# Optimization experiments

Hardware: AMD Instinct MI355X
Metric: run time of the kernel (lower is better)

The kernel has to match this reference:

```python
import jax, jax.numpy as jnp
import numpy as np
import math

B, H, L, D = 2, 16, 2048, 128

def setup_inputs() -> dict:
    key = jax.random.key(0)
    kq, kk, kv, km = jax.random.split(key, 4)
    q = jax.random.normal(kq, (B, H, L, D), dtype=jnp.float32)
    k = jax.random.normal(kk, (B, H, L, D), dtype=jnp.float32)
    v = jax.random.normal(kv, (B, H, L, D), dtype=jnp.float32)
    mask = jax.random.randint(km, (B, 1, L, L), 0, 2, dtype=jnp.int32)
    return {"q": q, "k": k, "v": v, "mask": mask}

def reference(q, k, v, mask):
    d_tensor = q.shape[-1]
    # ReLU applied to V before attention (the custom twist)
    v = jax.nn.relu(v)
    # score = q @ k^T / sqrt(d)  -> [B,H,L,L]
    score = jnp.einsum('bhqd,bhkd->bhqk', q, k) / math.sqrt(d_tensor)
    score = jnp.where(mask == 0, jnp.float32(-10000.0), score)
    attn = jax.nn.softmax(score, axis=-1)
    # result = attn @ relu(v) -> [B,H,L,D]
    return jnp.einsum('bhqk,bhkd->bhqd', attn, v)
```

## Files before the change

### kernel.cpp

```cpp
#include <hip/hip_runtime.h>
#include <hip/hip_bf16.h>
#include <math.h>

typedef __attribute__((ext_vector_type(8)))  short short8;
typedef __attribute__((ext_vector_type(16))) float f32x16;

#define Bc    2
#define Hc    16
#define Lc    2048
#define Dc    128
#define QBLK  128
#define KBLK  64
#define LOG2E 1.4426950408889634f
#define SCALE 0.08838834764831845f
#define SCL2  (SCALE * LOG2E)

#define KB_OFF   0u
#define KB_BYTES (32u * 2048u * 128u * 2u)
#define VT_OFF   (KB_OFF + KB_BYTES)
#define VT_BYTES (32u * 2048u * 128u * 2u)
#define MB_OFF   (VT_OFF + VT_BYTES)

__device__ __forceinline__ unsigned pk2(float a, float b) {
    unsigned short ua = __builtin_bit_cast(unsigned short, __float2bfloat16(a));
    unsigned short ub = __builtin_bit_cast(unsigned short, __float2bfloat16(b));
    return (unsigned)ua | ((unsigned)ub << 16);
}
__device__ __forceinline__ unsigned short bf16b(float a) {
    return __builtin_bit_cast(unsigned short, __float2bfloat16(a));
}
__device__ __forceinline__ void gload_lds16(const void* g, void* l) {
    __builtin_amdgcn_global_load_lds(
        (const __attribute__((address_space(1))) unsigned int*)g,
        (__attribute__((address_space(3))) unsigned int*)l, 16, 0, 0);
}
__device__ __forceinline__ unsigned cvtpk(float lo, float hi) {
    unsigned r;
    asm("v_cvt_pk_bf16_f32 %0, %1, %2" : "=v"(r) : "v"(lo), "v"(hi));
    return r;
}

__global__ void conv_k_kernel(const float* __restrict__ k, unsigned short* __restrict__ kb) {
    int idx8 = blockIdx.x * 256 + threadIdx.x;
    size_t base = (size_t)idx8 * 8;
    float4 f0 = *(const float4*)(k + base);
    float4 f1 = *(const float4*)(k + base + 4);
    uint4 w;
    w.x = pk2(f0.x, f0.y); w.y = pk2(f0.z, f0.w);
    w.z = pk2(f1.x, f1.y); w.w = pk2(f1.z, f1.w);
    *(uint4*)(kb + base) = w;
}

__global__ void transp_v_kernel(const float* __restrict__ v, unsigned short* __restrict__ vt) {
    __shared__ float t[32][33];
    int d0 = blockIdx.x * 32;
    int l0 = blockIdx.y * 32;
    int bh = blockIdx.z;
    int tx = threadIdx.x, ty = threadIdx.y;
    const float* src = v + (size_t)bh * Lc * Dc;
    unsigned short* dst = vt + (size_t)bh * Dc * Lc;
    #pragma unroll
    for (int i = 0; i < 4; ++i) {
        int row = ty * 4 + i;
        t[row][tx] = fmaxf(src[(size_t)(l0 + row) * Dc + d0 + tx], 0.f);
    }
    __syncthreads();
    #pragma unroll
    for (int i = 0; i < 4; ++i) {
        int drow = ty * 4 + i;
        dst[(size_t)(d0 + drow) * Lc + l0 + tx] = bf16b(t[tx][drow]);
    }
}

__global__ void mask_pack_kernel(const int* __restrict__ mask, unsigned long long* __restrict__ mb) {
    int tid  = threadIdx.x;
    int wv   = blockIdx.x * 4 + (tid >> 6);
    int lane = tid & 63;
    int b    = wv >> 16;
    int l    = (wv >> 5) & 2047;
    int ktw  = wv & 31;
    int m = mask[(((size_t)(b * 2048 + l)) << 11) + ktw * 64 + lane];
    unsigned long long bal = __ballot(m != 0);
    if (lane == 0) mb[(((size_t)(b * 32 + ktw)) << 11) + l] = bal;
}

__global__ __launch_bounds__(256, 2) void rev_attn_kernel(
    const float* __restrict__ q,
    const unsigned short* __restrict__ kb,
    const unsigned short* __restrict__ vt,
    const unsigned long long* __restrict__ mb,
    float* __restrict__ out)
{
    __shared__ __align__(16) char smem[65536];

    const int tid  = threadIdx.x;
    const int w    = tid >> 6;
    const int lane = tid & 63;
    const int l31  = lane & 31;
    const int hi   = lane >> 5;
    const int bh   = blockIdx.y;
    const int b    = bh >> 4;
    const int qb   = blockIdx.x * QBLK + w * 32;
    const int qrow = qb + l31;

    const float*              qp = q  + (size_t)bh * Lc * Dc;
    const unsigned short*     kp = kb + (size_t)bh * Lc * Dc;
    const unsigned short*     vp = vt + (size_t)bh * Dc * Lc;
    const unsigned long long* mp = mb + ((size_t)b << 16);
    float*                    op = out + (size_t)bh * Lc * Dc;

    short8 qf[8];
    {
        const float* qr0 = qp + (size_t)qrow * Dc + hi * 8;
        #pragma unroll
        for (int c = 0; c < 8; ++c) {
            const float* src = qr0 + c * 16;
            #pragma unroll
            for (int j = 0; j < 8; ++j)
                qf[c][j] = (short)bf16b(src[j] * SCL2);
        }
    }

    f32x16 o0 = (f32x16)0.f, o1 = (f32x16)0.f, o2 = (f32x16)0.f, o3 = (f32x16)0.f;
    f32x16 lacc = (f32x16)0.f;
    short8 ones;
    #pragma unroll
    for (int j = 0; j < 8; ++j) ones[j] = (short)0x3F80;

    #define STAGE(buf, kt_) do {                                                   \
        char* Kdst = smem + (buf) * 16384;                                         \
        char* Vdst = smem + 32768 + (buf) * 16384;                                 \
        _Pragma("unroll")                                                          \
        for (int p = 0; p < 4; ++p) {                                              \
            int l   = p * 256 + tid;                                               \
            int row = l >> 4, cl = l & 15;                                         \
            int s_  = cl ^ (row & 15);                                             \
            gload_lds16(kp + (size_t)((kt_) + row) * Dc + s_ * 8, Kdst + l * 16);  \
            int ds_ = row + ((s_ >> 3) << 6);                                      \
            int ko_ = (s_ & 7) * 8;                                                \
            gload_lds16(vp + (size_t)ds_ * Lc + (kt_) + ko_, Vdst + l * 16);       \
        }                                                                          \
    } while (0)

    int cur = 0;
    STAGE(0, 0);
    __syncthreads();

    for (int kt = 0; kt < Lc; kt += KBLK) {
        if (kt + KBLK < Lc) STAGE(cur ^ 1, kt + KBLK);
        unsigned long long mw = mp[((size_t)(kt >> 6) << 11) + qrow];
        const char* Kb = smem + cur * 16384;
        const char* Vb = smem + 32768 + cur * 16384;

        f32x16 s0 = (f32x16)0.f, s1 = (f32x16)0.f;
        __builtin_amdgcn_s_setprio(1);
        #pragma unroll
        for (int c = 0; c < 8; ++c) {
            int r0 = l31;
            short8 kf0 = *(const short8*)(Kb + r0 * 256 + ((((c << 1) | hi)) ^ (r0 & 15)) * 16);
            s0 = __builtin_amdgcn_mfma_f32_32x32x16_bf16(kf0, qf[c], s0, 0, 0, 0);
            int r1 = 32 + l31;
            short8 kf1 = *(const short8*)(Kb + r1 * 256 + ((((c << 1) | hi)) ^ (r1 & 15)) * 16);
            s1 = __builtin_amdgcn_mfma_f32_32x32x16_bf16(kf1, qf[c], s1, 0, 0, 0);
        }
        __builtin_amdgcn_s_setprio(0);

        unsigned m0 = ((unsigned)(mw & 0xffffffffull)) >> (4 * hi);
        unsigned m1 = ((unsigned)(mw >> 32)) >> (4 * hi);
        #pragma unroll
        for (int r = 0; r < 16; ++r) {
            const int cs = (r & 3) + 8 * (r >> 2);
            float e0 = exp2f(s0[r]);
            float e1 = exp2f(s1[r]);
            s0[r] = ((m0 >> cs) & 1u) ? e0 : 0.f;
            s1[r] = ((m1 >> cs) & 1u) ? e1 : 0.f;
        }

        short8 pa[4];
        {
            union { unsigned u[4]; short8 v; } t0, t1, t2, t3;
            unsigned a, a2, bb, b2;
            a  = cvtpk(s0[0], s0[1]);  a2 = cvtpk(s0[2], s0[3]);
            bb = cvtpk(s0[4], s0[5]);  b2 = cvtpk(s0[6], s0[7]);
            asm volatile("v_permlane32_swap_b32 %0, %1" : "+v"(a),  "+v"(bb));
            asm volatile("v_permlane32_swap_b32 %0, %1" : "+v"(a2), "+v"(b2));
            t0.u[0] = a; t0.u[1] = a2; t0.u[2] = bb; t0.u[3] = b2;
            a  = cvtpk(s0[8],  s0[9]);  a2 = cvtpk(s0[10], s0[11]);
            bb = cvtpk(s0[12], s0[13]); b2 = cvtpk(s0[14], s0[15]);
            asm volatile("v_permlane32_swap_b32 %0, %1" : "+v"(a),  "+v"(bb));
            asm volatile("v_permlane32_swap_b32 %0, %1" : "+v"(a2), "+v"(b2));
            t1.u[0] = a; t1.u[1] = a2; t1.u[2] = bb; t1.u[3] = b2;
            a  = cvtpk(s1[0], s1[1]);  a2 = cvtpk(s1[2], s1[3]);
            bb = cvtpk(s1[4], s1[5]);  b2 = cvtpk(s1[6], s1[7]);
            asm volatile("v_permlane32_swap_b32 %0, %1" : "+v"(a),  "+v"(bb));
            asm volatile("v_permlane32_swap_b32 %0, %1" : "+v"(a2), "+v"(b2));
            t2.u[0] = a; t2.u[1] = a2; t2.u[2] = bb; t2.u[3] = b2;
            a  = cvtpk(s1[8],  s1[9]);  a2 = cvtpk(s1[10], s1[11]);
            bb = cvtpk(s1[12], s1[13]); b2 = cvtpk(s1[14], s1[15]);
            asm volatile("v_permlane32_swap_b32 %0, %1" : "+v"(a),  "+v"(bb));
            asm volatile("v_permlane32_swap_b32 %0, %1" : "+v"(a2), "+v"(b2));
            t3.u[0] = a; t3.u[1] = a2; t3.u[2] = bb; t3.u[3] = b2;
            pa[0] = t0.v; pa[1] = t1.v; pa[2] = t2.v; pa[3] = t3.v;
        }

        __builtin_amdgcn_s_setprio(1);
        #pragma unroll
        for (int ks = 0; ks < 4; ++ks)
            lacc = __builtin_amdgcn_mfma_f32_32x32x16_bf16(ones, pa[ks], lacc, 0, 0, 0);
        #pragma unroll
        for (int dt = 0; dt < 4; ++dt) {
            int vrow = (dt & 1) * 32 + l31;
            int hs   = dt >> 1;
            int vswz = vrow & 15;
            f32x16 acc = (dt == 0) ? o0 : (dt == 1) ? o1 : (dt == 2) ? o2 : o3;
            #pragma unroll
            for (int ks = 0; ks < 4; ++ks) {
                int off = vrow * 256 + (((hs << 3) | (ks << 1) | hi) ^ vswz) * 16;
                short8 vf = *(const short8*)(Vb + off);
                acc = __builtin_amdgcn_mfma_f32_32x32x16_bf16(vf, pa[ks], acc, 0, 0, 0);
            }
            if (dt == 0) o0 = acc; else if (dt == 1) o1 = acc; else if (dt == 2) o2 = acc; else o3 = acc;
        }
        __builtin_amdgcn_s_setprio(0);

        __syncthreads();
        cur ^= 1;
    }

    __syncthreads();
    float inv = 1.0f / lacc[0];
    float* scr = (float*)(smem + w * 4608);
    const int qq = lane >> 1;
    const int dh = (lane & 1) * 16;
    #pragma unroll
    for (int dt = 0; dt < 4; ++dt) {
        const f32x16& oo = (dt == 0) ? o0 : (dt == 1) ? o1 : (dt == 2) ? o2 : o3;
        #pragma unroll
        for (int r = 0; r < 16; ++r) {
            int drow = (r & 3) + 8 * (r >> 2) + 4 * hi;
            scr[drow * 36 + l31] = oo[r] * inv;
        }
        asm volatile("s_waitcnt lgkmcnt(0)" ::: "memory");
        __builtin_amdgcn_sched_barrier(0);
        float t[16];
        #pragma unroll
        for (int c2 = 0; c2 < 16; ++c2)
            t[c2] = scr[(dh + c2) * 36 + qq];
        asm volatile("s_waitcnt lgkmcnt(0)" ::: "memory");
        __builtin_amdgcn_sched_barrier(0);
        float* od = op + (size_t)(qb + qq) * Dc + dt * 32 + dh;
        #pragma unroll
        for (int c2 = 0; c2 < 4; ++c2) {
            float4 f4; f4.x = t[c2*4]; f4.y = t[c2*4+1]; f4.z = t[c2*4+2]; f4.w = t[c2*4+3];
            *(float4*)(od + c2 * 4) = f4;
        }
    }
}

extern "C" void kernel_launch(void* const* d_in, const int* in_sizes, int n_in,
                              void* d_out, int out_size, void* d_ws, size_t ws_size,
                              hipStream_t stream) {
    const float* q    = (const float*)d_in[0];
    const float* k    = (const float*)d_in[1];
    const float* v    = (const float*)d_in[2];
    const int*   mask = (const int*)d_in[3];
    float*       out  = (float*)d_out;

    char* ws = (char*)d_ws;
    unsigned short*     kb  = (unsigned short*)(ws + KB_OFF);
    unsigned short*     vt  = (unsigned short*)(ws + VT_OFF);
    unsigned long long* mbp = (unsigned long long*)(ws + MB_OFF);

    hipLaunchKernelGGL(conv_k_kernel, dim3(4096), dim3(256), 0, stream, k, kb);
    hipLaunchKernelGGL(transp_v_kernel, dim3(4, 64, 32), dim3(32, 8), 0, stream, v, vt);
    hipLaunchKernelGGL(mask_pack_kernel, dim3(32768), dim3(256), 0, stream, mask, mbp);

    hipLaunchKernelGGL(rev_attn_kernel, dim3(Lc / QBLK, Bc * Hc), dim3(256), 0, stream,
                       q, kb, vt, mbp, out);
}
```

Baseline: 130.9 us.

## Split each key tile across wave pairs and compute row sums with VALU

Each block now runs 512 threads (8 waves). Pairs of waves share the same 32 query rows, and each wave handles one 32-key half of every 64-key tile, for both QK^T and PV. The row-sum MFMA against a ones vector is replaced by VALU adds plus a cross-half shuffle. At the end, partial O and l are combined through LDS before normalisation and the store. The aim is more waves in flight for latency hiding and shorter per-wave dependency chains. The cost is an extra LDS reduction with several block barriers, and register pressure from the tighter launch bounds.

New measurement: 244.0 us. 1.86x slower.

```diff
diff --git a/kernel.cpp b/kernel.cpp
--- a/kernel.cpp
+++ b/kernel.cpp
@@ -84,7 +84,7 @@
     if (lane == 0) mb[(((size_t)(b * 32 + ktw)) << 11) + l] = bal;
 }
 
-__global__ __launch_bounds__(256, 2) void rev_attn_kernel(
+__global__ __launch_bounds__(512, 4) void rev_attn_kernel(
     const float* __restrict__ q,
     const unsigned short* __restrict__ kb,
     const unsigned short* __restrict__ vt,
@@ -98,10 +98,12 @@
     const int lane = tid & 63;
     const int l31  = lane & 31;
     const int hi   = lane >> 5;
+    const int qg   = w >> 1;
+    const int kh   = w & 1;
     const int bh   = blockIdx.y;
     const int b    = bh >> 4;
-    const int qb   = blockIdx.x * QBLK + w * 32;
-    const int qrow = qb + l31;
+    const int qb   = blockIdx.x * QBLK;
+    const int qrow = qb + qg * 32 + l31;
 
     const float*              qp = q  + (size_t)bh * Lc * Dc;
     const unsigned short*     kp = kb + (size_t)bh * Lc * Dc;
@@ -122,17 +124,14 @@
     }
 
     f32x16 o0 = (f32x16)0.f, o1 = (f32x16)0.f, o2 = (f32x16)0.f, o3 = (f32x16)0.f;
-    f32x16 lacc = (f32x16)0.f;
-    short8 ones;
-    #pragma unroll
-    for (int j = 0; j < 8; ++j) ones[j] = (short)0x3F80;
+    float lrun = 0.f;
 
     #define STAGE(buf, kt_) do {                                                   \
         char* Kdst = smem + (buf) * 16384;                                         \
         char* Vdst = smem + 32768 + (buf) * 16384;                                 \
         _Pragma("unroll")                                                          \
-        for (int p = 0; p < 4; ++p) {                                              \
-            int l   = p * 256 + tid;                                               \
+        for (int p = 0; p < 2; ++p) {                                              \
+            int l   = p * 512 + tid;                                               \
             int row = l >> 4, cl = l & 15;                                         \
             int s_  = cl ^ (row & 15);                                             \
             gload_lds16(kp + (size_t)((kt_) + row) * Dc + s_ * 8, Kdst + l * 16);  \
@@ -146,67 +145,59 @@
     STAGE(0, 0);
     __syncthreads();
 
+    const int r0 = kh * 32 + l31;
     for (int kt = 0; kt < Lc; kt += KBLK) {
         if (kt + KBLK < Lc) STAGE(cur ^ 1, kt + KBLK);
         unsigned long long mw = mp[((size_t)(kt >> 6) << 11) + qrow];
         const char* Kb = smem + cur * 16384;
         const char* Vb = smem + 32768 + cur * 16384;
 
-        f32x16 s0 = (f32x16)0.f, s1 = (f32x16)0.f;
+        f32x16 s = (f32x16)0.f;
         __builtin_amdgcn_s_setprio(1);
         #pragma unroll
         for (int c = 0; c < 8; ++c) {
-            int r0 = l31;
-            short8 kf0 = *(const short8*)(Kb + r0 * 256 + ((((c << 1) | hi)) ^ (r0 & 15)) * 16);
-            s0 = __builtin_amdgcn_mfma_f32_32x32x16_bf16(kf0, qf[c], s0, 0, 0, 0);
-            int r1 = 32 + l31;
-            short8 kf1 = *(const short8*)(Kb + r1 * 256 + ((((c << 1) | hi)) ^ (r1 & 15)) * 16);
-            s1 = __builtin_amdgcn_mfma_f32_32x32x16_bf16(kf1, qf[c], s1, 0, 0, 0);
+            short8 kf = *(const short8*)(Kb + r0 * 256 + ((((c << 1) | hi)) ^ (r0 & 15)) * 16);
+            s = __builtin_amdgcn_mfma_f32_32x32x16_bf16(kf, qf[c], s, 0, 0, 0);
         }
         __builtin_amdgcn_s_setprio(0);
 
-        unsigned m0 = ((unsigned)(mw & 0xffffffffull)) >> (4 * hi);
-        unsigned m1 = ((unsigned)(mw >> 32)) >> (4 * hi);
+        unsigned mh = (unsigned)(mw >> (kh * 32));
+        unsigned m0 = mh >> (4 * hi);
         #pragma unroll
         for (int r = 0; r < 16; ++r) {
             const int cs = (r & 3) + 8 * (r >> 2);
-            float e0 = exp2f(s0[r]);
-            float e1 = exp2f(s1[r]);
-            s0[r] = ((m0 >> cs) & 1u) ? e0 : 0.f;
-            s1[r] = ((m1 >> cs) & 1u) ? e1 : 0.f;
-        }
-
-        short8 pa[4];
+            float e = exp2f(s[r]);
+            s[r] = ((m0 >> cs) & 1u) ? e : 0.f;
+        }
+
         {
-            union { unsigned u[4]; short8 v; } t0, t1, t2, t3;
+            float a0 = (s[0] + s[1]) + (s[2] + s[3]);
+            float a1 = (s[4] + s[5]) + (s[6] + s[7]);
+            float a2 = (s[8] + s[9]) + (s[10] + s[11]);
+            float a3 = (s[12] + s[13]) + (s[14] + s[15]);
+            float rs = (a0 + a1) + (a2 + a3);
+            rs += __shfl_xor(rs, 32);
+            lrun += rs;
+        }
+
+        short8 pa[2];
+        {
+            union { unsigned u[4]; short8 v; } t0, t1;
             unsigned a, a2, bb, b2;
-            a  = cvtpk(s0[0], s0[1]);  a2 = cvtpk(s0[2], s0[3]);
-            bb = cvtpk(s0[4], s0[5]);  b2 = cvtpk(s0[6], s0[7]);
+            a  = cvtpk(s[0], s[1]);  a2 = cvtpk(s[2], s[3]);
+            bb = cvtpk(s[4], s[5]);  b2 = cvtpk(s[6], s[7]);
             asm volatile("v_permlane32_swap_b32 %0, %1" : "+v"(a),  "+v"(bb));
             asm volatile("v_permlane32_swap_b32 %0, %1" : "+v"(a2), "+v"(b2));
             t0.u[0] = a; t0.u[1] = a2; t0.u[2] = bb; t0.u[3] = b2;
-            a  = cvtpk(s0[8],  s0[9]);  a2 = cvtpk(s0[10], s0[11]);
-            bb = cvtpk(s0[12], s0[13]); b2 = cvtpk(s0[14], s0[15]);
+            a  = cvtpk(s[8],  s[9]);  a2 = cvtpk(s[10], s[11]);
+            bb = cvtpk(s[12], s[13]); b2 = cvtpk(s[14], s[15]);
             asm volatile("v_permlane32_swap_b32 %0, %1" : "+v"(a),  "+v"(bb));
             asm volatile("v_permlane32_swap_b32 %0, %1" : "+v"(a2), "+v"(b2));
             t1.u[0] = a; t1.u[1] = a2; t1.u[2] = bb; t1.u[3] = b2;
-            a  = cvtpk(s1[0], s1[1]);  a2 = cvtpk(s1[2], s1[3]);
-            bb = cvtpk(s1[4], s1[5]);  b2 = cvtpk(s1[6], s1[7]);
-            asm volatile("v_permlane32_swap_b32 %0, %1" : "+v"(a),  "+v"(bb));
-            asm volatile("v_permlane32_swap_b32 %0, %1" : "+v"(a2), "+v"(b2));
-            t2.u[0] = a; t2.u[1] = a2; t2.u[2] = bb; t2.u[3] = b2;
-            a  = cvtpk(s1[8],  s1[9]);  a2 = cvtpk(s1[10], s1[11]);
-            bb = cvtpk(s1[12], s1[13]); b2 = cvtpk(s1[14], s1[15]);
-            asm volatile("v_permlane32_swap_b32 %0, %1" : "+v"(a),  "+v"(bb));
-            asm volatile("v_permlane32_swap_b32 %0, %1" : "+v"(a2), "+v"(b2));
-            t3.u[0] = a; t3.u[1] = a2; t3.u[2] = bb; t3.u[3] = b2;
-            pa[0] = t0.v; pa[1] = t1.v; pa[2] = t2.v; pa[3] = t3.v;
+            pa[0] = t0.v; pa[1] = t1.v;
         }
 
         __builtin_amdgcn_s_setprio(1);
-        #pragma unroll
-        for (int ks = 0; ks < 4; ++ks)
-            lacc = __builtin_amdgcn_mfma_f32_32x32x16_bf16(ones, pa[ks], lacc, 0, 0, 0);
         #pragma unroll
         for (int dt = 0; dt < 4; ++dt) {
             int vrow = (dt & 1) * 32 + l31;
@@ -214,9 +205,9 @@
             int vswz = vrow & 15;
             f32x16 acc = (dt == 0) ? o0 : (dt == 1) ? o1 : (dt == 2) ? o2 : o3;
             #pragma unroll
-            for (int ks = 0; ks < 4; ++ks) {
-                int off = vrow * 256 + (((hs << 3) | (ks << 1) | hi) ^ vswz) * 16;
-                short8 vf = *(const short8*)(Vb + off);
+            for (int ks = 0; ks < 2; ++ks) {
+                int colsel = (hs << 3) | (kh << 2) | (ks << 1) | hi;
+                short8 vf = *(const short8*)(Vb + vrow * 256 + ((colsel ^ vswz) * 16));
                 acc = __builtin_amdgcn_mfma_f32_32x32x16_bf16(vf, pa[ks], acc, 0, 0, 0);
             }
             if (dt == 0) o0 = acc; else if (dt == 1) o1 = acc; else if (dt == 2) o2 = acc; else o3 = acc;
@@ -227,33 +218,41 @@
         cur ^= 1;
     }
 
-    __syncthreads();
-    float inv = 1.0f / lacc[0];
-    float* scr = (float*)(smem + w * 4608);
-    const int qq = lane >> 1;
-    const int dh = (lane & 1) * 16;
+    float* scr = (float*)(smem + qg * 4096);
+    float* lsp = (float*)(smem + 16384 + qg * 128);
+    if (kh == 1 && hi == 0) lsp[l31] = lrun;
+    float inv = 0.f;
+    const int qq2 = kh * 16 + (lane >> 2);
+    const int dh2 = (lane & 3) * 8;
     #pragma unroll
     for (int dt = 0; dt < 4; ++dt) {
         const f32x16& oo = (dt == 0) ? o0 : (dt == 1) ? o1 : (dt == 2) ? o2 : o3;
-        #pragma unroll
-        for (int r = 0; r < 16; ++r) {
-            int drow = (r & 3) + 8 * (r >> 2) + 4 * hi;
-            scr[drow * 36 + l31] = oo[r] * inv;
-        }
-        asm volatile("s_waitcnt lgkmcnt(0)" ::: "memory");
-        __builtin_amdgcn_sched_barrier(0);
-        float t[16];
-        #pragma unroll
-        for (int c2 = 0; c2 < 16; ++c2)
-            t[c2] = scr[(dh + c2) * 36 + qq];
-        asm volatile("s_waitcnt lgkmcnt(0)" ::: "memory");
-        __builtin_amdgcn_sched_barrier(0);
-        float* od = op + (size_t)(qb + qq) * Dc + dt * 32 + dh;
-        #pragma unroll
-        for (int c2 = 0; c2 < 4; ++c2) {
-            float4 f4; f4.x = t[c2*4]; f4.y = t[c2*4+1]; f4.z = t[c2*4+2]; f4.w = t[c2*4+3];
-            *(float4*)(od + c2 * 4) = f4;
-        }
+        if (kh == 1) {
+            #pragma unroll
+            for (int r = 0; r < 16; ++r)
+                scr[((r & 3) + 8 * (r >> 2) + 4 * hi) * 32 + l31] = oo[r];
+        }
+        __syncthreads();
+        if (kh == 0) {
+            if (dt == 0) inv = 1.0f / (lrun + lsp[l31]);
+            #pragma unroll
+            for (int r = 0; r < 16; ++r) {
+                int ix = ((r & 3) + 8 * (r >> 2) + 4 * hi) * 32 + l31;
+                scr[ix] = (scr[ix] + oo[r]) * inv;
+            }
+        }
+        __syncthreads();
+        float t[8];
+        #pragma unroll
+        for (int c2 = 0; c2 < 8; ++c2)
+            t[c2] = scr[(dh2 + c2) * 32 + qq2];
+        float* od = op + (size_t)(qb + qg * 32 + qq2) * Dc + dt * 32 + dh2;
+        float4 f4a, f4b;
+        f4a.x = t[0]; f4a.y = t[1]; f4a.z = t[2]; f4a.w = t[3];
+        f4b.x = t[4]; f4b.y = t[5]; f4b.z = t[6]; f4b.w = t[7];
+        *(float4*)(od)     = f4a;
+        *(float4*)(od + 4) = f4b;
+        if (dt < 3) __syncthreads();
     }
 }
 
@@ -275,6 +274,6 @@
     hipLaunchKernelGGL(transp_v_kernel, dim3(4, 64, 32), dim3(32, 8), 0, stream, v, vt);
     hipLaunchKernelGGL(mask_pack_kernel, dim3(32768), dim3(256), 0, stream, mask, mbp);
 
-    hipLaunchKernelGGL(rev_attn_kernel, dim3(Lc / QBLK, Bc * Hc), dim3(256), 0, stream,
+    hipLaunchKernelGGL(rev_attn_kernel, dim3(Lc / QBLK, Bc * Hc), dim3(512), 0, stream,
                        q, kb, vt, mbp, out);
 }
```
